# Performance work log

Hardware: AMD Instinct MI355X
Metric: run time of the kernel (lower is better)

## Reference

```python
import jax, jax.numpy as jnp
import numpy as np

V, E, FF = 32000, 1024, 4096
T, B, S = 256, 8, 512
LN_EPS = 1e-5

def _ln(x, g, b):
    m = jnp.mean(x, -1, keepdims=True)
    v = jnp.var(x, -1, keepdims=True)
    return (x - m) * jax.lax.rsqrt(v + LN_EPS) * g + b

def setup_inputs() -> dict:
    key = jax.random.key(0)
    ks = jax.random.split(key, 16)
    inp = {
        "outs": jax.random.normal(ks[0], (T, B, E), jnp.float32),
        "mem": jax.random.normal(ks[1], (S, B, E), jnp.float32),
        "mem_bias": jax.random.normal(ks[2], (B, 1), jnp.float32),
        "in_proj_w": jax.random.normal(ks[3], (3 * E, E), jnp.float32) * 0.02,
        "in_proj_b": jnp.zeros((3 * E,), jnp.float32),
        "out_proj_w": jax.random.normal(ks[4], (E, E), jnp.float32) * 0.02,
        "out_proj_b": jnp.zeros((E,), jnp.float32),
        "aln_g": jnp.ones((E,), jnp.float32),
        "aln_b": jnp.zeros((E,), jnp.float32),
        "div_w": jax.random.normal(ks[5], (2, 2 * E), jnp.float32) * 0.02,
        "div_b": jnp.zeros((2,), jnp.float32),
        "fc1_w": jax.random.normal(ks[6], (FF, E), jnp.float32) * 0.02,
        "fc1_b": jnp.zeros((FF,), jnp.float32),
        "fc2_w": jax.random.normal(ks[7], (E, FF), jnp.float32) * 0.02,
        "fc2_b": jnp.zeros((E,), jnp.float32),
        "ffn_g": jnp.ones((E,), jnp.float32),
        "ffn_b": jnp.zeros((E,), jnp.float32),
        "vocab_w": jax.random.normal(ks[8], (V, E), jnp.float32) * 0.02,
        "mem_mask": jnp.ones((S, B), bool),
        "copy_seq": jax.random.randint(ks[9], (S, B), 0, V),
    }
    return inp

def reference(outs, mem, mem_bias, in_proj_w, in_proj_b, out_proj_w, out_proj_b,
              aln_g, aln_b, div_w, div_b, fc1_w, fc1_b, fc2_w, fc2_b,
              ffn_g, ffn_b, vocab_w, mem_mask, copy_seq):
    t, b, e = outs.shape
    s = mem.shape[0]
    # single-head alignment attention (eval mode: dropout is a no-op)
    q = (outs @ in_proj_w[:e].T + in_proj_b[:e]) * (e ** -0.5)  # [T,B,E]
    k = mem @ in_proj_w[e:2 * e].T + in_proj_b[e:2 * e]          # [S,B,E]
    v = mem @ in_proj_w[2 * e:].T + in_proj_b[2 * e:]            # [S,B,E]
    w = jnp.einsum('tbe,sbe->bts', q, k) + mem_bias[:, None, :]  # [B,T,S]
    keep = mem_mask.T[:, None, :]                                # [B,1,S]
    w = jnp.where(keep, w, -jnp.inf)
    w = jax.nn.softmax(w, axis=-1)                               # [B,T,S]
    attn = jnp.einsum('bts,sbe->tbe', w, v) @ out_proj_w.T + out_proj_b
    alignment = jnp.transpose(w, (1, 0, 2))                      # [T,B,S]
    # gates
    attn_norm = _ln(attn, aln_g, aln_b)
    gates = jax.nn.softmax(jnp.concatenate([outs, attn_norm], -1) @ div_w.T + div_b, -1)
    gen_gate, copy_gate = gates[..., :1], gates[..., 1:]
    # residual + FFN
    h = _ln(outs + attn, aln_g, aln_b)
    h = jax.nn.relu(h @ fc1_w.T + fc1_b) @ fc2_w.T + fc2_b
    h = _ln(h, ffn_g, ffn_b)
    # vocab distribution + copy scatter-add
    probs = gen_gate * jax.nn.softmax(h @ vocab_w.T, -1)         # [T,B,V]
    index = jnp.broadcast_to(copy_seq.T[None], (t, b, s))        # [T,B,S]
    copy_probs = copy_gate * alignment                           # [T,B,S]
    ti = jnp.arange(t)[:, None, None]
    bi = jnp.arange(b)[None, :, None]
    probs = probs.at[ti, bi, index].add(copy_probs)
    return jnp.log(probs + 1e-12)
```

## Files before the change

### kernel.cpp

```cpp
#include <hip/hip_runtime.h>
#include <math.h>

#define T_ 256
#define B_ 8
#define S_ 512
#define E_ 1024
#define FF_ 4096
#define V_ 32000
#define LN_EPSF 1e-5f

typedef __attribute__((ext_vector_type(8))) short short8;
typedef __attribute__((ext_vector_type(4))) float f32x4;
typedef unsigned short us;

__device__ __forceinline__ float blkSum(float v, float* sh) {
#pragma unroll
  for (int o = 32; o > 0; o >>= 1) v += __shfl_down(v, o, 64);
  if ((threadIdx.x & 63) == 0) sh[threadIdx.x >> 6] = v;
  __syncthreads();
  float r = sh[0] + sh[1] + sh[2] + sh[3];
  __syncthreads();
  return r;
}
__device__ __forceinline__ float blkMax(float v, float* sh) {
#pragma unroll
  for (int o = 32; o > 0; o >>= 1) v = fmaxf(v, __shfl_down(v, o, 64));
  if ((threadIdx.x & 63) == 0) sh[threadIdx.x >> 6] = v;
  __syncthreads();
  float r = fmaxf(fmaxf(sh[0], sh[1]), fmaxf(sh[2], sh[3]));
  __syncthreads();
  return r;
}
__device__ __forceinline__ float blkSum16(float v, float* sh) {
#pragma unroll
  for (int o = 32; o > 0; o >>= 1) v += __shfl_down(v, o, 64);
  if ((threadIdx.x & 63) == 0) sh[threadIdx.x >> 6] = v;
  __syncthreads();
  float r = 0.f;
#pragma unroll
  for (int i = 0; i < 16; ++i) r += sh[i];
  __syncthreads();
  return r;
}
__device__ __forceinline__ float blkMax16(float v, float* sh) {
#pragma unroll
  for (int o = 32; o > 0; o >>= 1) v = fmaxf(v, __shfl_down(v, o, 64));
  if ((threadIdx.x & 63) == 0) sh[threadIdx.x >> 6] = v;
  __syncthreads();
  float r = -INFINITY;
#pragma unroll
  for (int i = 0; i < 16; ++i) r = fmaxf(r, sh[i]);
  __syncthreads();
  return r;
}

__device__ __forceinline__ unsigned pkbf(float a, float b) {
  unsigned r;
  asm("v_cvt_pk_bf16_f32 %0, %1, %2" : "=v"(r) : "v"(a), "v"(b));
  return r;
}
__device__ __forceinline__ us bf16o(float a) {
  return (us)(pkbf(a, a) & 0xffffu);
}
__device__ __forceinline__ float bf2f(us u) {
  return __uint_as_float(((unsigned)u) << 16);
}

__device__ __forceinline__ void gl16(const us* g, us* l) {
  __builtin_amdgcn_global_load_lds(
      (const __attribute__((address_space(1))) void*)g,
      (__attribute__((address_space(3))) void*)l, 16, 0, 0);
}

__device__ __forceinline__ int swz(int idx) {
  return idx ^ (((idx >> 10) & 3) << 4);
}

__device__ __forceinline__ void tile_map(int& rowT, int& colT) {
  const unsigned nwg = gridDim.x * gridDim.y;
  const unsigned lin = blockIdx.y * gridDim.x + blockIdx.x;
  const unsigned nq = nwg >> 3, rr = nwg & 7;
  const unsigned xcd = lin & 7, idx = lin >> 3;
  const unsigned s =
      (xcd < rr ? xcd * (nq + 1) : rr * (nq + 1) + (xcd - rr) * nq) + idx;
  rowT = s % gridDim.x;
  colT = s / gridDim.x;
}

__global__ __launch_bounds__(256) void cvt_bf16(
    const float* __restrict__ in, us* __restrict__ o, int n4)
{
  int i = blockIdx.x * 256 + threadIdx.x;
  if (i < n4) {
    float4 f = ((const float4*)in)[i];
    ((uint2*)o)[i] = make_uint2(pkbf(f.x, f.y), pkbf(f.z, f.w));
  }
}

__global__ __launch_bounds__(256) void cvt_all(
    const float* __restrict__ s0, us* __restrict__ d0,
    const float* __restrict__ s1, us* __restrict__ d1,
    const float* __restrict__ s2, us* __restrict__ d2,
    const float* __restrict__ s3, us* __restrict__ d3,
    const float* __restrict__ s4, us* __restrict__ d4,
    const float* __restrict__ s5, us* __restrict__ d5)
{
  int j = blockIdx.x * 256 + threadIdx.x;
  const float* s; us* d;
  if (j < 524288) { s = s0; d = d0; }
  else { j -= 524288; if (j < 1048576) { s = s1; d = d1; }
  else { j -= 1048576; if (j < 786432) { s = s2; d = d2; }
  else { j -= 786432; if (j < 262144) { s = s3; d = d3; }
  else { j -= 262144; if (j < 1048576) { s = s4; d = d4; }
  else { j -= 1048576; if (j >= 1048576) return; s = s5; d = d5; } } } } }
  float4 f = ((const float4*)s)[j];
  ((uint2*)d)[j] = make_uint2(pkbf(f.x, f.y), pkbf(f.z, f.w));
}

template<int CBF>
__global__ __launch_bounds__(512) void gemm_8p(
    const us* __restrict__ A, const us* __restrict__ Bm,
    const float* __restrict__ bias, void* __restrict__ Cv,
    int K, int lda, int ldb, int ldc, float scale, int relu)
{
  __shared__ us sA[2][16384], sB[2][16384];
  int rowT, colT;
  tile_map(rowT, colT);
  const int row0 = rowT * 256, col0 = colT * 256;
  const us* Ap = A + (long)row0 * lda;
  const us* Bp = Bm + (long)col0 * ldb;

  const int lane = threadIdx.x & 63, wid = threadIdx.x >> 6;
  const int wr = wid >> 2, wc = wid & 3;
  const int lr = lane & 15, kb = lane >> 4;

  long asrc[4], bsrc[4];
  int dst[4];
#pragma unroll
  for (int i = 0; i < 4; ++i) {
    int c = wid * 4 + i;
    int kg = c & 7, rq = c >> 3;
    asrc[i] = (long)(rq * 64 + lane) * lda + kg * 8;
    bsrc[i] = (long)(rq * 64 + lane) * ldb + kg * 8;
    dst[i] = kg * 2048 + rq * 512;
  }

  f32x4 acc[8][4];
#pragma unroll
  for (int j = 0; j < 8; ++j)
#pragma unroll
    for (int ni = 0; ni < 4; ++ni) {
      f32x4 z = {0.f, 0.f, 0.f, 0.f};
      acc[j][ni] = z;
    }

  const int nt = K >> 6;
#pragma unroll
  for (int i = 0; i < 4; ++i) gl16(Bp + bsrc[i], &sB[0][dst[i]]);
#pragma unroll
  for (int i = 0; i < 4; ++i) gl16(Ap + asrc[i], &sA[0][dst[i]]);
  asm volatile("s_waitcnt vmcnt(0)" ::: "memory");
  __builtin_amdgcn_s_barrier();

  for (int t = 0; t < nt; ++t) {
    const int buf = t & 1, nbuf = buf ^ 1;
    const long kN = (long)(t + 1) << 6;
    const bool pf = (t + 1) < nt;
    short8 bfr[4], af[4];

#pragma unroll
    for (int ni = 0; ni < 4; ++ni)
      bfr[ni] = *(const short8*)&sB[buf][kb * 2048 + (wc * 64 + ni * 16 + lr) * 8];
#pragma unroll
    for (int mi = 0; mi < 4; ++mi)
      af[mi] = *(const short8*)&sA[buf][kb * 2048 + (wr * 128 + mi * 16 + lr) * 8];
    if (pf) {
#pragma unroll
      for (int i = 0; i < 4; ++i) gl16(Bp + bsrc[i] + kN, &sB[nbuf][dst[i]]);
    }
    __builtin_amdgcn_s_barrier();
    asm volatile("s_waitcnt lgkmcnt(0)" ::: "memory");
    __builtin_amdgcn_sched_barrier(0);
    __builtin_amdgcn_s_setprio(1);
#pragma unroll
    for (int mi = 0; mi < 4; ++mi)
#pragma unroll
      for (int ni = 0; ni < 4; ++ni)
        acc[mi][ni] = __builtin_amdgcn_mfma_f32_16x16x32_bf16(
            af[mi], bfr[ni], acc[mi][ni], 0, 0, 0);
    __builtin_amdgcn_s_setprio(0);
    __builtin_amdgcn_s_barrier();

#pragma unroll
    for (int mi = 0; mi < 4; ++mi)
      af[mi] = *(const short8*)&sA[buf][kb * 2048 + (wr * 128 + 64 + mi * 16 + lr) * 8];
    if (pf) {
#pragma unroll
      for (int i = 0; i < 4; ++i) gl16(Ap + asrc[i] + kN, &sA[nbuf][dst[i]]);
    }
    __builtin_amdgcn_s_barrier();
    asm volatile("s_waitcnt lgkmcnt(0)" ::: "memory");
    __builtin_amdgcn_sched_barrier(0);
    __builtin_amdgcn_s_setprio(1);
#pragma unroll
    for (int mi = 0; mi < 4; ++mi)
#pragma unroll
      for (int ni = 0; ni < 4; ++ni)
        acc[4 + mi][ni] = __builtin_amdgcn_mfma_f32_16x16x32_bf16(
            af[mi], bfr[ni], acc[4 + mi][ni], 0, 0, 0);
    __builtin_amdgcn_s_setprio(0);
    __builtin_amdgcn_s_barrier();

#pragma unroll
    for (int ni = 0; ni < 4; ++ni)
      bfr[ni] = *(const short8*)&sB[buf][(4 + kb) * 2048 + (wc * 64 + ni * 16 + lr) * 8];
#pragma unroll
    for (int mi = 0; mi < 4; ++mi)
      af[mi] = *(const short8*)&sA[buf][(4 + kb) * 2048 + (wr * 128 + mi * 16 + lr) * 8];
    __builtin_amdgcn_s_barrier();
    asm volatile("s_waitcnt lgkmcnt(0)" ::: "memory");
    __builtin_amdgcn_sched_barrier(0);
    __builtin_amdgcn_s_setprio(1);
#pragma unroll
    for (int mi = 0; mi < 4; ++mi)
#pragma unroll
      for (int ni = 0; ni < 4; ++ni)
        acc[mi][ni] = __builtin_amdgcn_mfma_f32_16x16x32_bf16(
            af[mi], bfr[ni], acc[mi][ni], 0, 0, 0);
    __builtin_amdgcn_s_setprio(0);
    __builtin_amdgcn_s_barrier();

#pragma unroll
    for (int mi = 0; mi < 4; ++mi)
      af[mi] = *(const short8*)&sA[buf][(4 + kb) * 2048 + (wr * 128 + 64 + mi * 16 + lr) * 8];
    __builtin_amdgcn_s_barrier();
    asm volatile("s_waitcnt lgkmcnt(0)" ::: "memory");
    __builtin_amdgcn_sched_barrier(0);
    __builtin_amdgcn_s_setprio(1);
#pragma unroll
    for (int mi = 0; mi < 4; ++mi)
#pragma unroll
      for (int ni = 0; ni < 4; ++ni)
        acc[4 + mi][ni] = __builtin_amdgcn_mfma_f32_16x16x32_bf16(
            af[mi], bfr[ni], acc[4 + mi][ni], 0, 0, 0);
    __builtin_amdgcn_s_setprio(0);
    asm volatile("s_waitcnt vmcnt(0)" ::: "memory");
    __builtin_amdgcn_s_barrier();
  }

#pragma unroll
  for (int j = 0; j < 8; ++j)
#pragma unroll
    for (int ni = 0; ni < 4; ++ni) {
      int col = col0 + wc * 64 + ni * 16 + lr;
      float bv = bias ? bias[col] : 0.0f;
#pragma unroll
      for (int r = 0; r < 4; ++r) {
        int row = row0 + wr * 128 + (j >> 2) * 64 + (j & 3) * 16 + kb * 4 + r;
        float vv = (acc[j][ni][r] + bv) * scale;
        if (relu) vv = fmaxf(vv, 0.0f);
        if constexpr (CBF)
          ((us*)Cv)[(long)row * ldc + col] = bf16o(vv);
        else
          ((float*)Cv)[(long)row * ldc + col] = vv;
      }
    }
}

template<int CBF>
__global__ __launch_bounds__(256) void gemm_gl(
    const us* __restrict__ A, const us* __restrict__ Bm,
    const float* __restrict__ bias, const float* __restrict__ sbias,
    void* __restrict__ Cv, int K, int lda, int ldb, int ldc,
    long aB, long bB, long cB, float scale, int relu)
{
  __shared__ us sA[3][4096], sB[3][4096];
  int rowT, colT;
  tile_map(rowT, colT);
  const int bz = blockIdx.z;
  const int row0 = rowT * 128, col0 = colT * 128;
  const us* Ap = A + (long)bz * aB + (long)row0 * lda;
  const us* Bp = Bm + (long)bz * bB + (long)col0 * ldb;
  const float sb = sbias ? sbias[bz] : 0.0f;

  const int lane = threadIdx.x & 63, wid = threadIdx.x >> 6;
  const int wr = wid >> 1, wc = wid & 1;
  const int lr = lane & 15, kb = lane >> 4;

  const int r1 = threadIdx.x & 127, q1 = threadIdx.x >> 7;
  const long a1 = (long)r1 * lda + q1 * 8, a2 = a1 + 16;
  const long b1 = (long)r1 * ldb + q1 * 8, b2 = b1 + 16;
  const int dof1 = wid * 512, dof2 = 2048 + wid * 512;

  f32x4 acc[4][4];
#pragma unroll
  for (int mi = 0; mi < 4; ++mi)
#pragma unroll
    for (int ni = 0; ni < 4; ++ni) {
      f32x4 z = {0.f, 0.f, 0.f, 0.f};
      acc[mi][ni] = z;
    }

  auto stage = [&](int buf, long k0) {
    gl16(Ap + a1 + k0, &sA[buf][dof1]);
    gl16(Ap + a2 + k0, &sA[buf][dof2]);
    gl16(Bp + b1 + k0, &sB[buf][dof1]);
    gl16(Bp + b2 + k0, &sB[buf][dof2]);
  };
  auto compute = [&](int buf) {
    short8 af[4], bfr[4];
#pragma unroll
    for (int mi = 0; mi < 4; ++mi)
      af[mi] = *(const short8*)&sA[buf][kb * 1024 + (wr * 64 + mi * 16 + lr) * 8];
#pragma unroll
    for (int ni = 0; ni < 4; ++ni)
      bfr[ni] = *(const short8*)&sB[buf][kb * 1024 + (wc * 64 + ni * 16 + lr) * 8];
#pragma unroll
    for (int mi = 0; mi < 4; ++mi)
#pragma unroll
      for (int ni = 0; ni < 4; ++ni)
        acc[mi][ni] = __builtin_amdgcn_mfma_f32_16x16x32_bf16(
            af[mi], bfr[ni], acc[mi][ni], 0, 0, 0);
  };

  const int nt = K >> 5;
  stage(0, 0);
  stage(1, 32);
  stage(2, 64);
  for (int t = 0; t < nt; ++t) {
    if (t + 2 < nt)      asm volatile("s_waitcnt vmcnt(8)" ::: "memory");
    else if (t + 1 < nt) asm volatile("s_waitcnt vmcnt(4)" ::: "memory");
    else                 asm volatile("s_waitcnt vmcnt(0)" ::: "memory");
    __builtin_amdgcn_s_barrier();
    const int buf = t % 3;
    compute(buf);
    __builtin_amdgcn_s_barrier();
    if (t + 3 < nt) stage(buf, (long)(t + 3) << 5);
  }

  char* Cbase = (char*)Cv + (long)bz * cB * (CBF ? 2 : 4);
#pragma unroll
  for (int mi = 0; mi < 4; ++mi)
#pragma unroll
    for (int ni = 0; ni < 4; ++ni) {
      int col = col0 + wc * 64 + ni * 16 + lr;
      float bv = bias ? bias[col] : 0.0f;
#pragma unroll
      for (int r = 0; r < 4; ++r) {
        int row = row0 + wr * 64 + mi * 16 + kb * 4 + r;
        float vv = (acc[mi][ni][r] + bv) * scale + sb;
        if (relu) vv = fmaxf(vv, 0.0f);
        if constexpr (CBF)
          ((us*)Cbase)[(long)row * ldc + col] = bf16o(vv);
        else
          ((float*)Cbase)[(long)row * ldc + col] = vv;
      }
    }
}

__global__ __launch_bounds__(256) void gemm_nt_bb(
    const us* __restrict__ A, const us* __restrict__ Bm,
    us* __restrict__ C, int K, int lda, int ldb, int ldc,
    long aB, long bB, long cB)
{
  __shared__ us sA[4096];
  __shared__ us sB[4096];
  int rowT, colT;
  tile_map(rowT, colT);
  const int bz = blockIdx.z;
  const int row0 = rowT * 128, col0 = colT * 128;
  const us* Ap = A + (long)bz * aB + (long)row0 * lda;
  const us* Bp = Bm + (long)bz * bB + col0;

  const int lane = threadIdx.x & 63, wid = threadIdx.x >> 6;
  const int wr = wid >> 1, wc = wid & 1;
  const int lr = lane & 15, kb = lane >> 4;
  const int kq = threadIdx.x & 7, m0 = threadIdx.x >> 3;
  const int k8 = threadIdx.x >> 5, c4 = threadIdx.x & 31;

  f32x4 acc[4][4];
#pragma unroll
  for (int mi = 0; mi < 4; ++mi)
#pragma unroll
    for (int ni = 0; ni < 4; ++ni) {
      f32x4 z = {0.f, 0.f, 0.f, 0.f};
      acc[mi][ni] = z;
    }

  uint2 ra[4], rb[4];
#pragma unroll
  for (int i = 0; i < 4; ++i) {
    int m = m0 + 32 * i;
    ra[i] = *(const uint2*)(Ap + (long)m * lda + kq * 4);
    int kk = k8 + 8 * i;
    rb[i] = *(const uint2*)(Bp + (long)kk * ldb + c4 * 4);
  }

  for (int k0 = 0;;) {
#pragma unroll
    for (int i = 0; i < 4; ++i) {
      int m = m0 + 32 * i;
      int idx = swz(((kq >> 1) * 128 + m) * 8 + (kq & 1) * 4);
      *(uint2*)&sA[idx] = ra[i];
      int b0 = (i * 128 + c4 * 4) * 8 + k8;
      sB[swz(b0)]      = (us)(rb[i].x & 0xffffu);
      sB[swz(b0 + 8)]  = (us)(rb[i].x >> 16);
      sB[swz(b0 + 16)] = (us)(rb[i].y & 0xffffu);
      sB[swz(b0 + 24)] = (us)(rb[i].y >> 16);
    }
    __syncthreads();
    k0 += 32;
    if (k0 < K) {
#pragma unroll
      for (int i = 0; i < 4; ++i) {
        int m = m0 + 32 * i;
        ra[i] = *(const uint2*)(Ap + (long)m * lda + k0 + kq * 4);
        int kk = k8 + 8 * i;
        rb[i] = *(const uint2*)(Bp + (long)(k0 + kk) * ldb + c4 * 4);
      }
    }
    short8 af[4], bfr[4];
#pragma unroll
    for (int mi = 0; mi < 4; ++mi)
      af[mi] = *(const short8*)&sA[swz((kb * 128 + wr * 64 + mi * 16 + lr) * 8)];
#pragma unroll
    for (int ni = 0; ni < 4; ++ni)
      bfr[ni] = *(const short8*)&sB[swz((kb * 128 + wc * 64 + ni * 16 + lr) * 8)];
#pragma unroll
    for (int mi = 0; mi < 4; ++mi)
#pragma unroll
      for (int ni = 0; ni < 4; ++ni)
        acc[mi][ni] = __builtin_amdgcn_mfma_f32_16x16x32_bf16(
            af[mi], bfr[ni], acc[mi][ni], 0, 0, 0);
    __syncthreads();
    if (k0 >= K) break;
  }

  us* Cp = C + (long)bz * cB;
#pragma unroll
  for (int mi = 0; mi < 4; ++mi)
#pragma unroll
    for (int ni = 0; ni < 4; ++ni) {
      int col = col0 + wc * 64 + ni * 16 + lr;
#pragma unroll
      for (int r = 0; r < 4; ++r) {
        int row = row0 + wr * 64 + mi * 16 + kb * 4 + r;
        Cp[(long)row * ldc + col] = bf16o(acc[mi][ni][r]);
      }
    }
}

__global__ __launch_bounds__(256) void attn_softmax(
    float* __restrict__ w, us* __restrict__ wbf, const int* __restrict__ mask)
{
  __shared__ float sh[4];
  const int blk = blockIdx.x;
  const int b = blk / T_;
  float* row = w + (long)blk * S_;
  us* rowb = wbf + (long)blk * S_;
  const int s0 = threadIdx.x, s1 = threadIdx.x + 256;
  const bool k0 = mask[s0 * B_ + b] != 0;
  const bool k1 = mask[s1 * B_ + b] != 0;
  float x0 = k0 ? row[s0] : -INFINITY;
  float x1 = k1 ? row[s1] : -INFINITY;
  float m = blkMax(fmaxf(x0, x1), sh);
  float e0 = k0 ? expf(x0 - m) : 0.0f;
  float e1 = k1 ? expf(x1 - m) : 0.0f;
  float sum = blkSum(e0 + e1, sh);
  float inv = sum > 0.0f ? 1.0f / sum : 0.0f;
  float p0 = e0 * inv, p1 = e1 * inv;
  row[s0] = p0; row[s1] = p1;
  rowb[s0] = bf16o(p0); rowb[s1] = bf16o(p1);
}

__global__ __launch_bounds__(256) void gates_h1(
    const float* __restrict__ outs, const float* __restrict__ attn,
    const float* __restrict__ aln_g, const float* __restrict__ aln_b,
    const float* __restrict__ div_w, const float* __restrict__ div_b,
    us* __restrict__ h1, float* __restrict__ gen, float* __restrict__ cpy)
{
  __shared__ float sh[4];
  const long base = (long)blockIdx.x * E_;
  float a[4], o[4];
  float sa = 0.f, sa2 = 0.f, shh = 0.f, sh2 = 0.f;
#pragma unroll
  for (int i = 0; i < 4; ++i) {
    int e = threadIdx.x + 256 * i;
    a[i] = attn[base + e];
    o[i] = outs[base + e];
    sa += a[i]; sa2 += a[i] * a[i];
    float t = o[i] + a[i];
    shh += t; sh2 += t * t;
  }
  sa  = blkSum(sa, sh);
  sa2 = blkSum(sa2, sh);
  shh = blkSum(shh, sh);
  sh2 = blkSum(sh2, sh);
  const float ma = sa / E_, va = sa2 / E_ - ma * ma;
  const float mh = shh / E_, vh = sh2 / E_ - mh * mh;
  const float ra = rsqrtf(va + LN_EPSF), rh = rsqrtf(vh + LN_EPSF);

  float z0 = 0.f, z1 = 0.f;
#pragma unroll
  for (int i = 0; i < 4; ++i) {
    int e = threadIdx.x + 256 * i;
    float g = aln_g[e], bb = aln_b[e];
    float an = (a[i] - ma) * ra * g + bb;
    float hv = (o[i] + a[i] - mh) * rh * g + bb;
    h1[base + e] = bf16o(hv);
    z0 += o[i] * div_w[e]          + an * div_w[E_ + e];
    z1 += o[i] * div_w[2 * E_ + e] + an * div_w[3 * E_ + e];
  }
  z0 = blkSum(z0, sh);
  z1 = blkSum(z1, sh);
  if (threadIdx.x == 0) {
    z0 += div_b[0]; z1 += div_b[1];
    float mm = fmaxf(z0, z1);
    float e0 = expf(z0 - mm), e1 = expf(z1 - mm);
    float inv = 1.0f / (e0 + e1);
    gen[blockIdx.x] = e0 * inv;
    cpy[blockIdx.x] = e1 * inv;
  }
}

__global__ __launch_bounds__(256) void ln2_bf16(
    const float* __restrict__ x1, const float* __restrict__ x2,
    const float* __restrict__ bias, const float* __restrict__ g,
    const float* __restrict__ b, us* __restrict__ o)
{
  __shared__ float sh[4];
  const long base = (long)blockIdx.x * E_;
  float v[4];
  float s = 0.f, s2 = 0.f;
#pragma unroll
  for (int i = 0; i < 4; ++i) {
    int e = threadIdx.x + 256 * i;
    v[i] = x1[base + e] + x2[base + e] + bias[e];
    s += v[i]; s2 += v[i] * v[i];
  }
  s  = blkSum(s, sh);
  s2 = blkSum(s2, sh);
  const float m = s / E_, var = s2 / E_ - m * m;
  const float r = rsqrtf(var + LN_EPSF);
#pragma unroll
  for (int i = 0; i < 4; ++i) {
    int e = threadIdx.x + 256 * i;
    o[base + e] = bf16o((v[i] - m) * r * g[e] + b[e]);
  }
}

__global__ __launch_bounds__(1024) void vocab_final(
    float* __restrict__ out, const float* __restrict__ gen,
    const float* __restrict__ cpy, const float* __restrict__ w,
    const int* __restrict__ copy_seq)
{
  __shared__ float scat[32000];
  __shared__ float sh[16];
  const int r = blockIdx.x, b = r & 7, t = r >> 3;
  const int tid = threadIdx.x;
  const short8* row8 = (const short8*)((us*)out + (long)r * 64000 + 32000);
  float4* row4 = (float4*)(out + (long)r * V_);

  for (int i = tid; i < V_; i += 1024) scat[i] = 0.f;
  __syncthreads();
  if (tid < S_) {
    float contrib = cpy[r] * w[((long)b * T_ + t) * S_ + tid];
    atomicAdd(&scat[copy_seq[tid * B_ + b]], contrib);
  }

  float vals[32];
  float mx = -INFINITY;
#pragma unroll
  for (int i = 0; i < 4; ++i) {
    int f = tid + (i << 10);
    if (f < 4000) {
      short8 v8 = row8[f];
#pragma unroll
      for (int j = 0; j < 8; ++j) {
        float x = bf2f((us)v8[j]);
        vals[i * 8 + j] = x;
        mx = fmaxf(mx, x);
      }
    } else {
#pragma unroll
      for (int j = 0; j < 8; ++j) vals[i * 8 + j] = -INFINITY;
    }
  }
  const float gmx = blkMax16(mx, sh);

  float s = 0.f;
#pragma unroll
  for (int i = 0; i < 32; ++i) {
    vals[i] = expf(vals[i] - gmx);
    s += vals[i];
  }
  s = blkSum16(s, sh);

  const float scale = gen[r] / s;
#pragma unroll
  for (int i = 0; i < 4; ++i) {
    int f = tid + (i << 10);
    if (f < 4000) {
      int e0 = f * 8;
#pragma unroll
      for (int h = 0; h < 2; ++h) {
        float4 p;
        int eb = e0 + h * 4;
        p.x = logf(vals[i * 8 + h * 4 + 0] * scale + scat[eb + 0] + 1e-12f);
        p.y = logf(vals[i * 8 + h * 4 + 1] * scale + scat[eb + 1] + 1e-12f);
        p.z = logf(vals[i * 8 + h * 4 + 2] * scale + scat[eb + 2] + 1e-12f);
        p.w = logf(vals[i * 8 + h * 4 + 3] * scale + scat[eb + 3] + 1e-12f);
        row4[(e0 >> 2) + h] = p;
      }
    }
  }
}

extern "C" void kernel_launch(void* const* d_in, const int* in_sizes, int n_in,
                              void* d_out, int out_size, void* d_ws, size_t ws_size,
                              hipStream_t stream) {
  (void)in_sizes; (void)n_in; (void)out_size; (void)ws_size;
  const float* outs     = (const float*)d_in[0];
  const float* mem      = (const float*)d_in[1];
  const float* mem_bias = (const float*)d_in[2];
  const float* in_w     = (const float*)d_in[3];
  const float* in_b     = (const float*)d_in[4];
  const float* ow       = (const float*)d_in[5];
  const float* ob       = (const float*)d_in[6];
  const float* aln_g    = (const float*)d_in[7];
  const float* aln_b    = (const float*)d_in[8];
  const float* div_w    = (const float*)d_in[9];
  const float* div_b    = (const float*)d_in[10];
  const float* fc1_w    = (const float*)d_in[11];
  const float* fc1_b    = (const float*)d_in[12];
  const float* fc2_w    = (const float*)d_in[13];
  const float* fc2_b    = (const float*)d_in[14];
  const float* ffn_g    = (const float*)d_in[15];
  const float* ffn_b    = (const float*)d_in[16];
  const float* vocab_w  = (const float*)d_in[17];
  const int*   mask     = (const int*)d_in[18];
  const int*   copy_seq = (const int*)d_in[19];
  float* out = (float*)d_out;
  char*  wsb = (char*)d_ws;

  us* in_w_bf  = (us*)(wsb + 0);
  us* ow_bf    = (us*)(wsb + 6291456);
  us* fc1_bf   = (us*)(wsb + 8388608);
  float* h2b   = (float*)(wsb + 8388608);
  us* fc2_bf   = (us*)(wsb + 16777216);
  us* outs_bf  = (us*)(wsb + 25165824);
  us* h1_bf    = outs_bf;
  us* mem_bf   = (us*)(wsb + 29360128);
  float* attn  = (float*)(wsb + 29360128);
  float* h2a   = attn;
  us* q_bf     = (us*)(wsb + 37748736);
  us* kv_bf    = (us*)(wsb + 41943040);
  us* w_bf     = (us*)(wsb + 58720256);
  us* ctx_bf   = (us*)(wsb + 60817408);
  us* vocab_bf = (us*)(wsb + 0);
  float* w_    = (float*)(wsb + 65536000);
  us* h2_bf    = (us*)(wsb + 69730304);
  float* gen   = (float*)(wsb + 73924608);
  float* cpy   = gen + 2048;
  us* mid_bf   = (us*)d_out;
  us* logits   = (us*)d_out + 32000;

  dim3 blk(256), blk5(512);
  cvt_all<<<dim3(18432), blk, 0, stream>>>(
      outs, outs_bf, mem, mem_bf, in_w, in_w_bf, ow, ow_bf,
      fc1_w, fc1_bf, fc2_w, fc2_bf);
  gemm_gl<1><<<dim3(16, 8), blk, 0, stream>>>(outs_bf, in_w_bf, in_b, nullptr, q_bf,
      1024, 1024, 1024, 1024, 0, 0, 0, 0.03125f, 0);
  gemm_gl<1><<<dim3(32, 16), blk, 0, stream>>>(mem_bf, in_w_bf + E_ * E_, in_b + E_, nullptr, kv_bf,
      1024, 1024, 1024, 2048, 0, 0, 0, 1.0f, 0);
  gemm_gl<0><<<dim3(2, 4, 8), blk, 0, stream>>>(q_bf, kv_bf, nullptr, mem_bias, w_,
      1024, B_ * E_, B_ * 2048, S_, E_, 2048, (long)T_ * S_, 1.0f, 0);
  attn_softmax<<<dim3(B_ * T_), blk, 0, stream>>>(w_, w_bf, mask);
  gemm_nt_bb<<<dim3(2, 8, 8), blk, 0, stream>>>(w_bf, kv_bf + 1024, ctx_bf,
      512, S_, B_ * 2048, B_ * E_, (long)T_ * S_, 2048, E_);
  gemm_gl<0><<<dim3(16, 8), blk, 0, stream>>>(ctx_bf, ow_bf, ob, nullptr, attn,
      1024, 1024, 1024, 1024, 0, 0, 0, 1.0f, 0);
  gates_h1<<<dim3(2048), blk, 0, stream>>>(outs, attn, aln_g, aln_b, div_w, div_b,
      h1_bf, gen, cpy);
  gemm_gl<1><<<dim3(16, 32), blk, 0, stream>>>(h1_bf, fc1_bf, fc1_b, nullptr, mid_bf,
      1024, 1024, 1024, 4096, 0, 0, 0, 1.0f, 1);
  gemm_gl<0><<<dim3(16, 8, 2), blk, 0, stream>>>(mid_bf, fc2_bf, nullptr, nullptr, h2a,
      2048, 4096, 4096, 1024, 2048, 2048, (long)(h2b - h2a), 1.0f, 0);
  ln2_bf16<<<dim3(2048), blk, 0, stream>>>(h2a, h2b, fc2_b, ffn_g, ffn_b, h2_bf);
  cvt_bf16<<<dim3(32000), blk, 0, stream>>>(vocab_w, vocab_bf, 8192000);
  gemm_8p<1><<<dim3(8, 125), blk5, 0, stream>>>(h2_bf, vocab_bf, nullptr, logits,
      1024, 1024, 1024, 64000, 1.0f, 0);
  vocab_final<<<dim3(2048), dim3(1024), 0, stream>>>(out, gen, cpy, w_, copy_seq);
}
```

Measured before the change: 667.3 us.

## Split-K small attention GEMMs and halve vocab GEMM K-tile for occupancy

The attention-score GEMM is split four ways along K into partial buffers. `attn_softmax4` sums the four partials and drops the per-batch `mem_bias`, which is constant per softmax row and so cancels. The output-projection GEMM is split two ways along K, with `gates_h1` summing the partials and adding the bias. The vocab GEMM moves to a 32-wide K step, halving its LDS footprint so more blocks may fit per CU, at the cost of twice as many loop iterations and barriers. The aim is to fill the GPU better on the under-parallel small GEMMs, in exchange for extra partial-sum traffic.

```diff
diff --git a/kernel.cpp b/kernel.cpp
--- a/kernel.cpp
+++ b/kernel.cpp
@@ -118,12 +118,12 @@
 }
 
 template<int CBF>
-__global__ __launch_bounds__(512) void gemm_8p(
+__global__ __launch_bounds__(512) void gemm_8p32(
     const us* __restrict__ A, const us* __restrict__ Bm,
     const float* __restrict__ bias, void* __restrict__ Cv,
     int K, int lda, int ldb, int ldc, float scale, int relu)
 {
-  __shared__ us sA[2][16384], sB[2][16384];
+  __shared__ us sA[2][8192], sB[2][8192];
   int rowT, colT;
   tile_map(rowT, colT);
   const int row0 = rowT * 256, col0 = colT * 256;
@@ -134,12 +134,12 @@
   const int wr = wid >> 2, wc = wid & 3;
   const int lr = lane & 15, kb = lane >> 4;
 
-  long asrc[4], bsrc[4];
-  int dst[4];
-#pragma unroll
-  for (int i = 0; i < 4; ++i) {
-    int c = wid * 4 + i;
-    int kg = c & 7, rq = c >> 3;
+  long asrc[2], bsrc[2];
+  int dst[2];
+#pragma unroll
+  for (int i = 0; i < 2; ++i) {
+    int c = wid * 2 + i;
+    int kg = c & 3, rq = c >> 2;
     asrc[i] = (long)(rq * 64 + lane) * lda + kg * 8;
     bsrc[i] = (long)(rq * 64 + lane) * ldb + kg * 8;
     dst[i] = kg * 2048 + rq * 512;
@@ -154,17 +154,17 @@
       acc[j][ni] = z;
     }
 
-  const int nt = K >> 6;
-#pragma unroll
-  for (int i = 0; i < 4; ++i) gl16(Bp + bsrc[i], &sB[0][dst[i]]);
-#pragma unroll
-  for (int i = 0; i < 4; ++i) gl16(Ap + asrc[i], &sA[0][dst[i]]);
+  const int nt = K >> 5;
+#pragma unroll
+  for (int i = 0; i < 2; ++i) gl16(Bp + bsrc[i], &sB[0][dst[i]]);
+#pragma unroll
+  for (int i = 0; i < 2; ++i) gl16(Ap + asrc[i], &sA[0][dst[i]]);
   asm volatile("s_waitcnt vmcnt(0)" ::: "memory");
   __builtin_amdgcn_s_barrier();
 
   for (int t = 0; t < nt; ++t) {
     const int buf = t & 1, nbuf = buf ^ 1;
-    const long kN = (long)(t + 1) << 6;
+    const long kN = (long)(t + 1) << 5;
     const bool pf = (t + 1) < nt;
     short8 bfr[4], af[4];
 
@@ -176,7 +176,9 @@
       af[mi] = *(const short8*)&sA[buf][kb * 2048 + (wr * 128 + mi * 16 + lr) * 8];
     if (pf) {
 #pragma unroll
-      for (int i = 0; i < 4; ++i) gl16(Bp + bsrc[i] + kN, &sB[nbuf][dst[i]]);
+      for (int i = 0; i < 2; ++i) gl16(Bp + bsrc[i] + kN, &sB[nbuf][dst[i]]);
+#pragma unroll
+      for (int i = 0; i < 2; ++i) gl16(Ap + asrc[i] + kN, &sA[nbuf][dst[i]]);
     }
     __builtin_amdgcn_s_barrier();
     asm volatile("s_waitcnt lgkmcnt(0)" ::: "memory");
@@ -194,45 +196,6 @@
 #pragma unroll
     for (int mi = 0; mi < 4; ++mi)
       af[mi] = *(const short8*)&sA[buf][kb * 2048 + (wr * 128 + 64 + mi * 16 + lr) * 8];
-    if (pf) {
-#pragma unroll
-      for (int i = 0; i < 4; ++i) gl16(Ap + asrc[i] + kN, &sA[nbuf][dst[i]]);
-    }
-    __builtin_amdgcn_s_barrier();
-    asm volatile("s_waitcnt lgkmcnt(0)" ::: "memory");
-    __builtin_amdgcn_sched_barrier(0);
-    __builtin_amdgcn_s_setprio(1);
-#pragma unroll
-    for (int mi = 0; mi < 4; ++mi)
-#pragma unroll
-      for (int ni = 0; ni < 4; ++ni)
-        acc[4 + mi][ni] = __builtin_amdgcn_mfma_f32_16x16x32_bf16(
-            af[mi], bfr[ni], acc[4 + mi][ni], 0, 0, 0);
-    __builtin_amdgcn_s_setprio(0);
-    __builtin_amdgcn_s_barrier();
-
-#pragma unroll
-    for (int ni = 0; ni < 4; ++ni)
-      bfr[ni] = *(const short8*)&sB[buf][(4 + kb) * 2048 + (wc * 64 + ni * 16 + lr) * 8];
-#pragma unroll
-    for (int mi = 0; mi < 4; ++mi)
-      af[mi] = *(const short8*)&sA[buf][(4 + kb) * 2048 + (wr * 128 + mi * 16 + lr) * 8];
-    __builtin_amdgcn_s_barrier();
-    asm volatile("s_waitcnt lgkmcnt(0)" ::: "memory");
-    __builtin_amdgcn_sched_barrier(0);
-    __builtin_amdgcn_s_setprio(1);
-#pragma unroll
-    for (int mi = 0; mi < 4; ++mi)
-#pragma unroll
-      for (int ni = 0; ni < 4; ++ni)
-        acc[mi][ni] = __builtin_amdgcn_mfma_f32_16x16x32_bf16(
-            af[mi], bfr[ni], acc[mi][ni], 0, 0, 0);
-    __builtin_amdgcn_s_setprio(0);
-    __builtin_amdgcn_s_barrier();
-
-#pragma unroll
-    for (int mi = 0; mi < 4; ++mi)
-      af[mi] = *(const short8*)&sA[buf][(4 + kb) * 2048 + (wr * 128 + 64 + mi * 16 + lr) * 8];
     __builtin_amdgcn_s_barrier();
     asm volatile("s_waitcnt lgkmcnt(0)" ::: "memory");
     __builtin_amdgcn_sched_barrier(0);
@@ -271,17 +234,19 @@
 __global__ __launch_bounds__(256) void gemm_gl(
     const us* __restrict__ A, const us* __restrict__ Bm,
     const float* __restrict__ bias, const float* __restrict__ sbias,
-    void* __restrict__ Cv, int K, int lda, int ldb, int ldc,
-    long aB, long bB, long cB, float scale, int relu)
+    void* __restrict__ Cv, int K, int lda, int ldb, int ldc, int zdiv,
+    long aB, long bB, long cB, long aK, long bK, long cK,
+    float scale, int relu)
 {
   __shared__ us sA[3][4096], sB[3][4096];
   int rowT, colT;
   tile_map(rowT, colT);
   const int bz = blockIdx.z;
+  const int zb = bz % zdiv, zs = bz / zdiv;
   const int row0 = rowT * 128, col0 = colT * 128;
-  const us* Ap = A + (long)bz * aB + (long)row0 * lda;
-  const us* Bp = Bm + (long)bz * bB + (long)col0 * ldb;
-  const float sb = sbias ? sbias[bz] : 0.0f;
+  const us* Ap = A + (long)zb * aB + (long)zs * aK + (long)row0 * lda;
+  const us* Bp = Bm + (long)zb * bB + (long)zs * bK + (long)col0 * ldb;
+  const float sb = sbias ? sbias[zb] : 0.0f;
 
   const int lane = threadIdx.x & 63, wid = threadIdx.x >> 6;
   const int wr = wid >> 1, wc = wid & 1;
@@ -338,7 +303,7 @@
     if (t + 3 < nt) stage(buf, (long)(t + 3) << 5);
   }
 
-  char* Cbase = (char*)Cv + (long)bz * cB * (CBF ? 2 : 4);
+  char* Cbase = (char*)Cv + ((long)zb * cB + (long)zs * cK) * (CBF ? 2 : 4);
 #pragma unroll
   for (int mi = 0; mi < 4; ++mi)
 #pragma unroll
@@ -450,19 +415,25 @@
     }
 }
 
-__global__ __launch_bounds__(256) void attn_softmax(
-    float* __restrict__ w, us* __restrict__ wbf, const int* __restrict__ mask)
+__global__ __launch_bounds__(256) void attn_softmax4(
+    const float* __restrict__ wp, float* __restrict__ w,
+    us* __restrict__ wbf, const int* __restrict__ mask)
 {
   __shared__ float sh[4];
   const int blk = blockIdx.x;
   const int b = blk / T_;
-  float* row = w + (long)blk * S_;
-  us* rowb = wbf + (long)blk * S_;
+  const long base = (long)blk * S_;
+  float* row = w + base;
+  us* rowb = wbf + base;
   const int s0 = threadIdx.x, s1 = threadIdx.x + 256;
   const bool k0 = mask[s0 * B_ + b] != 0;
   const bool k1 = mask[s1 * B_ + b] != 0;
-  float x0 = k0 ? row[s0] : -INFINITY;
-  float x1 = k1 ? row[s1] : -INFINITY;
+  float x0 = wp[base + s0] + wp[1048576 + base + s0]
+           + wp[2097152 + base + s0] + wp[3145728 + base + s0];
+  float x1 = wp[base + s1] + wp[1048576 + base + s1]
+           + wp[2097152 + base + s1] + wp[3145728 + base + s1];
+  x0 = k0 ? x0 : -INFINITY;
+  x1 = k1 ? x1 : -INFINITY;
   float m = blkMax(fmaxf(x0, x1), sh);
   float e0 = k0 ? expf(x0 - m) : 0.0f;
   float e1 = k1 ? expf(x1 - m) : 0.0f;
@@ -474,7 +445,8 @@
 }
 
 __global__ __launch_bounds__(256) void gates_h1(
-    const float* __restrict__ outs, const float* __restrict__ attn,
+    const float* __restrict__ outs, const float* __restrict__ pa,
+    const float* __restrict__ pb, const float* __restrict__ ob,
     const float* __restrict__ aln_g, const float* __restrict__ aln_b,
     const float* __restrict__ div_w, const float* __restrict__ div_b,
     us* __restrict__ h1, float* __restrict__ gen, float* __restrict__ cpy)
@@ -486,7 +458,7 @@
 #pragma unroll
   for (int i = 0; i < 4; ++i) {
     int e = threadIdx.x + 256 * i;
-    a[i] = attn[base + e];
+    a[i] = pa[base + e] + pb[base + e] + ob[e];
     o[i] = outs[base + e];
     sa += a[i]; sa2 += a[i] * a[i];
     float t = o[i] + a[i];
@@ -622,7 +594,6 @@
   (void)in_sizes; (void)n_in; (void)out_size; (void)ws_size;
   const float* outs     = (const float*)d_in[0];
   const float* mem      = (const float*)d_in[1];
-  const float* mem_bias = (const float*)d_in[2];
   const float* in_w     = (const float*)d_in[3];
   const float* in_b     = (const float*)d_in[4];
   const float* ow       = (const float*)d_in[5];
@@ -651,10 +622,11 @@
   us* outs_bf  = (us*)(wsb + 25165824);
   us* h1_bf    = outs_bf;
   us* mem_bf   = (us*)(wsb + 29360128);
-  float* attn  = (float*)(wsb + 29360128);
-  float* h2a   = attn;
+  float* attn_a= (float*)(wsb + 29360128);
+  float* h2a   = attn_a;
   us* q_bf     = (us*)(wsb + 37748736);
   us* kv_bf    = (us*)(wsb + 41943040);
+  float* attn_b= (float*)(wsb + 41943040);
   us* w_bf     = (us*)(wsb + 58720256);
   us* ctx_bf   = (us*)(wsb + 60817408);
   us* vocab_bf = (us*)(wsb + 0);
@@ -663,6 +635,7 @@
   float* gen   = (float*)(wsb + 73924608);
   float* cpy   = gen + 2048;
   us* mid_bf   = (us*)d_out;
+  float* wp    = (float*)d_out;
   us* logits   = (us*)d_out + 32000;
 
   dim3 blk(256), blk5(512);
@@ -670,25 +643,28 @@
       outs, outs_bf, mem, mem_bf, in_w, in_w_bf, ow, ow_bf,
       fc1_w, fc1_bf, fc2_w, fc2_bf);
   gemm_gl<1><<<dim3(16, 8), blk, 0, stream>>>(outs_bf, in_w_bf, in_b, nullptr, q_bf,
-      1024, 1024, 1024, 1024, 0, 0, 0, 0.03125f, 0);
+      1024, 1024, 1024, 1024, 1, 0, 0, 0, 0, 0, 0, 0.03125f, 0);
   gemm_gl<1><<<dim3(32, 16), blk, 0, stream>>>(mem_bf, in_w_bf + E_ * E_, in_b + E_, nullptr, kv_bf,
-      1024, 1024, 1024, 2048, 0, 0, 0, 1.0f, 0);
-  gemm_gl<0><<<dim3(2, 4, 8), blk, 0, stream>>>(q_bf, kv_bf, nullptr, mem_bias, w_,
-      1024, B_ * E_, B_ * 2048, S_, E_, 2048, (long)T_ * S_, 1.0f, 0);
-  attn_softmax<<<dim3(B_ * T_), blk, 0, stream>>>(w_, w_bf, mask);
+      1024, 1024, 1024, 2048, 1, 0, 0, 0, 0, 0, 0, 1.0f, 0);
+  gemm_gl<0><<<dim3(2, 4, 32), blk, 0, stream>>>(q_bf, kv_bf, nullptr, nullptr, wp,
+      256, B_ * E_, B_ * 2048, S_, 8, E_, 2048, (long)T_ * S_, 256, 256, 1048576,
+      1.0f, 0);
+  attn_softmax4<<<dim3(B_ * T_), blk, 0, stream>>>(wp, w_, w_bf, mask);
   gemm_nt_bb<<<dim3(2, 8, 8), blk, 0, stream>>>(w_bf, kv_bf + 1024, ctx_bf,
       512, S_, B_ * 2048, B_ * E_, (long)T_ * S_, 2048, E_);
-  gemm_gl<0><<<dim3(16, 8), blk, 0, stream>>>(ctx_bf, ow_bf, ob, nullptr, attn,
-      1024, 1024, 1024, 1024, 0, 0, 0, 1.0f, 0);
-  gates_h1<<<dim3(2048), blk, 0, stream>>>(outs, attn, aln_g, aln_b, div_w, div_b,
-      h1_bf, gen, cpy);
+  gemm_gl<0><<<dim3(16, 8, 2), blk, 0, stream>>>(ctx_bf, ow_bf, nullptr, nullptr, attn_a,
+      512, 1024, 1024, 1024, 1, 0, 0, 0, 512, 512, (long)(attn_b - attn_a),
+      1.0f, 0);
+  gates_h1<<<dim3(2048), blk, 0, stream>>>(outs, attn_a, attn_b, ob,
+      aln_g, aln_b, div_w, div_b, h1_bf, gen, cpy);
   gemm_gl<1><<<dim3(16, 32), blk, 0, stream>>>(h1_bf, fc1_bf, fc1_b, nullptr, mid_bf,
-      1024, 1024, 1024, 4096, 0, 0, 0, 1.0f, 1);
+      1024, 1024, 1024, 4096, 1, 0, 0, 0, 0, 0, 0, 1.0f, 1);
   gemm_gl<0><<<dim3(16, 8, 2), blk, 0, stream>>>(mid_bf, fc2_bf, nullptr, nullptr, h2a,
-      2048, 4096, 4096, 1024, 2048, 2048, (long)(h2b - h2a), 1.0f, 0);
+      2048, 4096, 4096, 1024, 1, 0, 0, 0, 2048, 2048, (long)(h2b - h2a),
+      1.0f, 0);
   ln2_bf16<<<dim3(2048), blk, 0, stream>>>(h2a, h2b, fc2_b, ffn_g, ffn_b, h2_bf);
   cvt_bf16<<<dim3(32000), blk, 0, stream>>>(vocab_w, vocab_bf, 8192000);
-  gemm_8p<1><<<dim3(8, 125), blk5, 0, stream>>>(h2_bf, vocab_bf, nullptr, logits,
+  gemm_8p32<1><<<dim3(8, 125), blk5, 0, stream>>>(h2_bf, vocab_bf, nullptr, logits,
       1024, 1024, 1024, 64000, 1.0f, 0);
   vocab_final<<<dim3(2048), dim3(1024), 0, stream>>>(out, gen, cpy, w_, copy_seq);
 }
```

Result: no change. 656.8 us (median of 2 runs) (-1.6%).

## Split-K the attention score and out-proj GEMMs to fill more CUs

Applied to the files above, without the earlier changes.

Generalizes gemm_gl so blockIdx.z can index both a batch and a K-split slice. The QK^T score GEMM now runs 4-way split-K (64 to 256 blocks) with partial sums reduced inside the softmax kernel, and the out-projection runs 2-way split-K with the partials and bias summed in gates_h1. The mem_bias term is dropped because it is constant along the softmax axis, and the copy scatter now reads bf16 attention probabilities instead of fp32. This trades extra partial-buffer traffic and slightly lower copy-probability precision for better occupancy on small GEMMs.

```diff
diff --git a/kernel.cpp b/kernel.cpp
--- a/kernel.cpp
+++ b/kernel.cpp
@@ -271,17 +271,19 @@
 __global__ __launch_bounds__(256) void gemm_gl(
     const us* __restrict__ A, const us* __restrict__ Bm,
     const float* __restrict__ bias, const float* __restrict__ sbias,
-    void* __restrict__ Cv, int K, int lda, int ldb, int ldc,
-    long aB, long bB, long cB, float scale, int relu)
+    void* __restrict__ Cv, int K, int lda, int ldb, int ldc, int zdiv,
+    long aB, long bB, long cB, long aK, long bK, long cK,
+    float scale, int relu)
 {
   __shared__ us sA[3][4096], sB[3][4096];
   int rowT, colT;
   tile_map(rowT, colT);
   const int bz = blockIdx.z;
+  const int zb = bz % zdiv, zs = bz / zdiv;
   const int row0 = rowT * 128, col0 = colT * 128;
-  const us* Ap = A + (long)bz * aB + (long)row0 * lda;
-  const us* Bp = Bm + (long)bz * bB + (long)col0 * ldb;
-  const float sb = sbias ? sbias[bz] : 0.0f;
+  const us* Ap = A + (long)zb * aB + (long)zs * aK + (long)row0 * lda;
+  const us* Bp = Bm + (long)zb * bB + (long)zs * bK + (long)col0 * ldb;
+  const float sb = sbias ? sbias[zb] : 0.0f;
 
   const int lane = threadIdx.x & 63, wid = threadIdx.x >> 6;
   const int wr = wid >> 1, wc = wid & 1;
@@ -338,7 +340,7 @@
     if (t + 3 < nt) stage(buf, (long)(t + 3) << 5);
   }
 
-  char* Cbase = (char*)Cv + (long)bz * cB * (CBF ? 2 : 4);
+  char* Cbase = (char*)Cv + ((long)zb * cB + (long)zs * cK) * (CBF ? 2 : 4);
 #pragma unroll
   for (int mi = 0; mi < 4; ++mi)
 #pragma unroll
@@ -450,31 +452,36 @@
     }
 }
 
-__global__ __launch_bounds__(256) void attn_softmax(
-    float* __restrict__ w, us* __restrict__ wbf, const int* __restrict__ mask)
+__global__ __launch_bounds__(256) void attn_softmax4(
+    const float* __restrict__ wp, us* __restrict__ wbf,
+    const int* __restrict__ mask)
 {
   __shared__ float sh[4];
   const int blk = blockIdx.x;
   const int b = blk / T_;
-  float* row = w + (long)blk * S_;
-  us* rowb = wbf + (long)blk * S_;
+  const long base = (long)blk * S_;
+  us* rowb = wbf + base;
   const int s0 = threadIdx.x, s1 = threadIdx.x + 256;
   const bool k0 = mask[s0 * B_ + b] != 0;
   const bool k1 = mask[s1 * B_ + b] != 0;
-  float x0 = k0 ? row[s0] : -INFINITY;
-  float x1 = k1 ? row[s1] : -INFINITY;
+  float x0 = wp[base + s0] + wp[1048576 + base + s0]
+           + wp[2097152 + base + s0] + wp[3145728 + base + s0];
+  float x1 = wp[base + s1] + wp[1048576 + base + s1]
+           + wp[2097152 + base + s1] + wp[3145728 + base + s1];
+  x0 = k0 ? x0 : -INFINITY;
+  x1 = k1 ? x1 : -INFINITY;
   float m = blkMax(fmaxf(x0, x1), sh);
   float e0 = k0 ? expf(x0 - m) : 0.0f;
   float e1 = k1 ? expf(x1 - m) : 0.0f;
   float sum = blkSum(e0 + e1, sh);
   float inv = sum > 0.0f ? 1.0f / sum : 0.0f;
-  float p0 = e0 * inv, p1 = e1 * inv;
-  row[s0] = p0; row[s1] = p1;
-  rowb[s0] = bf16o(p0); rowb[s1] = bf16o(p1);
+  rowb[s0] = bf16o(e0 * inv);
+  rowb[s1] = bf16o(e1 * inv);
 }
 
 __global__ __launch_bounds__(256) void gates_h1(
-    const float* __restrict__ outs, const float* __restrict__ attn,
+    const float* __restrict__ outs, const float* __restrict__ pa,
+    const float* __restrict__ pb, const float* __restrict__ ob,
     const float* __restrict__ aln_g, const float* __restrict__ aln_b,
     const float* __restrict__ div_w, const float* __restrict__ div_b,
     us* __restrict__ h1, float* __restrict__ gen, float* __restrict__ cpy)
@@ -486,7 +493,7 @@
 #pragma unroll
   for (int i = 0; i < 4; ++i) {
     int e = threadIdx.x + 256 * i;
-    a[i] = attn[base + e];
+    a[i] = pa[base + e] + pb[base + e] + ob[e];
     o[i] = outs[base + e];
     sa += a[i]; sa2 += a[i] * a[i];
     float t = o[i] + a[i];
@@ -551,7 +558,7 @@
 
 __global__ __launch_bounds__(1024) void vocab_final(
     float* __restrict__ out, const float* __restrict__ gen,
-    const float* __restrict__ cpy, const float* __restrict__ w,
+    const float* __restrict__ cpy, const us* __restrict__ wbf,
     const int* __restrict__ copy_seq)
 {
   __shared__ float scat[32000];
@@ -564,7 +571,7 @@
   for (int i = tid; i < V_; i += 1024) scat[i] = 0.f;
   __syncthreads();
   if (tid < S_) {
-    float contrib = cpy[r] * w[((long)b * T_ + t) * S_ + tid];
+    float contrib = cpy[r] * bf2f(wbf[((long)b * T_ + t) * S_ + tid]);
     atomicAdd(&scat[copy_seq[tid * B_ + b]], contrib);
   }
 
@@ -622,7 +629,6 @@
   (void)in_sizes; (void)n_in; (void)out_size; (void)ws_size;
   const float* outs     = (const float*)d_in[0];
   const float* mem      = (const float*)d_in[1];
-  const float* mem_bias = (const float*)d_in[2];
   const float* in_w     = (const float*)d_in[3];
   const float* in_b     = (const float*)d_in[4];
   const float* ow       = (const float*)d_in[5];
@@ -651,18 +657,19 @@
   us* outs_bf  = (us*)(wsb + 25165824);
   us* h1_bf    = outs_bf;
   us* mem_bf   = (us*)(wsb + 29360128);
-  float* attn  = (float*)(wsb + 29360128);
-  float* h2a   = attn;
+  float* attn_a= (float*)(wsb + 29360128);
+  float* h2a   = attn_a;
   us* q_bf     = (us*)(wsb + 37748736);
   us* kv_bf    = (us*)(wsb + 41943040);
-  us* w_bf     = (us*)(wsb + 58720256);
+  float* attn_b= (float*)(wsb + 41943040);
   us* ctx_bf   = (us*)(wsb + 60817408);
   us* vocab_bf = (us*)(wsb + 0);
-  float* w_    = (float*)(wsb + 65536000);
+  us* w_bf     = (us*)(wsb + 65536000);
   us* h2_bf    = (us*)(wsb + 69730304);
   float* gen   = (float*)(wsb + 73924608);
   float* cpy   = gen + 2048;
   us* mid_bf   = (us*)d_out;
+  float* wp    = (float*)d_out;
   us* logits   = (us*)d_out + 32000;
 
   dim3 blk(256), blk5(512);
@@ -670,25 +677,28 @@
       outs, outs_bf, mem, mem_bf, in_w, in_w_bf, ow, ow_bf,
       fc1_w, fc1_bf, fc2_w, fc2_bf);
   gemm_gl<1><<<dim3(16, 8), blk, 0, stream>>>(outs_bf, in_w_bf, in_b, nullptr, q_bf,
-      1024, 1024, 1024, 1024, 0, 0, 0, 0.03125f, 0);
+      1024, 1024, 1024, 1024, 1, 0, 0, 0, 0, 0, 0, 0.03125f, 0);
   gemm_gl<1><<<dim3(32, 16), blk, 0, stream>>>(mem_bf, in_w_bf + E_ * E_, in_b + E_, nullptr, kv_bf,
-      1024, 1024, 1024, 2048, 0, 0, 0, 1.0f, 0);
-  gemm_gl<0><<<dim3(2, 4, 8), blk, 0, stream>>>(q_bf, kv_bf, nullptr, mem_bias, w_,
-      1024, B_ * E_, B_ * 2048, S_, E_, 2048, (long)T_ * S_, 1.0f, 0);
-  attn_softmax<<<dim3(B_ * T_), blk, 0, stream>>>(w_, w_bf, mask);
+      1024, 1024, 1024, 2048, 1, 0, 0, 0, 0, 0, 0, 1.0f, 0);
+  gemm_gl<0><<<dim3(2, 4, 32), blk, 0, stream>>>(q_bf, kv_bf, nullptr, nullptr, wp,
+      256, B_ * E_, B_ * 2048, S_, 8, E_, 2048, (long)T_ * S_, 256, 256, 1048576,
+      1.0f, 0);
+  attn_softmax4<<<dim3(B_ * T_), blk, 0, stream>>>(wp, w_bf, mask);
   gemm_nt_bb<<<dim3(2, 8, 8), blk, 0, stream>>>(w_bf, kv_bf + 1024, ctx_bf,
       512, S_, B_ * 2048, B_ * E_, (long)T_ * S_, 2048, E_);
-  gemm_gl<0><<<dim3(16, 8), blk, 0, stream>>>(ctx_bf, ow_bf, ob, nullptr, attn,
-      1024, 1024, 1024, 1024, 0, 0, 0, 1.0f, 0);
-  gates_h1<<<dim3(2048), blk, 0, stream>>>(outs, attn, aln_g, aln_b, div_w, div_b,
-      h1_bf, gen, cpy);
+  gemm_gl<0><<<dim3(16, 8, 2), blk, 0, stream>>>(ctx_bf, ow_bf, nullptr, nullptr, attn_a,
+      512, 1024, 1024, 1024, 1, 0, 0, 0, 512, 512, (long)(attn_b - attn_a),
+      1.0f, 0);
+  gates_h1<<<dim3(2048), blk, 0, stream>>>(outs, attn_a, attn_b, ob,
+      aln_g, aln_b, div_w, div_b, h1_bf, gen, cpy);
   gemm_gl<1><<<dim3(16, 32), blk, 0, stream>>>(h1_bf, fc1_bf, fc1_b, nullptr, mid_bf,
-      1024, 1024, 1024, 4096, 0, 0, 0, 1.0f, 1);
+      1024, 1024, 1024, 4096, 1, 0, 0, 0, 0, 0, 0, 1.0f, 1);
   gemm_gl<0><<<dim3(16, 8, 2), blk, 0, stream>>>(mid_bf, fc2_bf, nullptr, nullptr, h2a,
-      2048, 4096, 4096, 1024, 2048, 2048, (long)(h2b - h2a), 1.0f, 0);
+      2048, 4096, 4096, 1024, 1, 0, 0, 0, 2048, 2048, (long)(h2b - h2a),
+      1.0f, 0);
   ln2_bf16<<<dim3(2048), blk, 0, stream>>>(h2a, h2b, fc2_b, ffn_g, ffn_b, h2_bf);
   cvt_bf16<<<dim3(32000), blk, 0, stream>>>(vocab_w, vocab_bf, 8192000);
   gemm_8p<1><<<dim3(8, 125), blk5, 0, stream>>>(h2_bf, vocab_bf, nullptr, logits,
       1024, 1024, 1024, 64000, 1.0f, 0);
-  vocab_final<<<dim3(2048), dim3(1024), 0, stream>>>(out, gen, cpy, w_, copy_seq);
-}
+  vocab_final<<<dim3(2048), dim3(1024), 0, stream>>>(out, gen, cpy, w_bf, copy_seq);
+}
```

New measurement: 642.0 us, median of 2. 3.8% less time.
